# Optimization experiments

Hardware: AMD Instinct MI355X
Metric: run time of the kernel (lower is better)

Reference implementation:

```python
import jax, jax.numpy as jnp
import numpy as np

NH = 5   # num_multiheads (forced by the 5 gamma parameters)
FH = 64  # filters_head == in_dim (forced by residual broadcast)


def setup_inputs() -> dict:
    key = jax.random.key(0)
    k1, k2, k3 = jax.random.split(key, 3)
    B, C, D, H, W = 4, FH, 8, 64, 64
    x = jax.random.normal(k1, (B, C, D, H, W), dtype=jnp.float32)
    # pointwise qkv projection (stand-in for RBF_modified2d): in_dim -> 3*NH*FH
    Wqkv = jax.random.normal(k2, (3 * NH * FH, C), dtype=jnp.float32) * 0.02
    bqkv = jnp.zeros((3 * NH * FH,), dtype=jnp.float32)
    # gammas init to zeros in torch; use random values so attention path contributes
    gamma = jax.random.uniform(k3, (NH,), dtype=jnp.float32)
    return {"x": x, "Wqkv": Wqkv, "bqkv": bqkv, "gamma": gamma}


def reference(x, Wqkv, bqkv, gamma):
    B, C, D, H, W = x.shape
    # pointwise projection: (B, 3*NH*FH, D, H, W)
    qkv = jnp.einsum('bcdhw,oc->bodhw', x, Wqkv) + bqkv[None, :, None, None, None]
    # 'b (nh c) d h w -> b nh c d h w' with c = 3*FH, then chunk into q,k,v
    qkv = qkv.reshape(B, NH, 3 * FH, D, H, W)
    q, k, v = qkv[:, :, :FH], qkv[:, :, FH:2 * FH], qkv[:, :, 2 * FH:]
    # sim = k @ q^T over the last two (spatial) dims: (b,nh,c,d,H,H)
    sim = jnp.einsum('bncdiw,bncdjw->bncdij', k, q)
    att = jax.nn.softmax(sim, axis=-1)
    # att @ v -> (b, nh, c, d, H, W)
    pv = jnp.einsum('bncdij,bncdjw->bncdiw', att, v)
    # rearrange 'b nh c d h w -> b (c nh) d h w'
    out_att = pv.transpose(0, 2, 1, 3, 4, 5).reshape(B, FH * NH, D, H, W)
    # chunk into NH heads along merged channel axis -> (B, NH, FH, D, H, W)
    heads = out_att.reshape(B, NH, FH, D, H, W)
    # stack([gamma_i * head_i + x for i]) -> (NH, B, C, D, H, W)
    result = gamma[None, :, None, None, None, None] * heads + x[:, None]
    # rearrange 'nh b c d h w -> b (c nh) d h w'
    result = result.transpose(0, 2, 1, 3, 4, 5)  # (B, C, NH, D, H, W)
    return result.reshape(B, C * NH, D, H, W)
```

## Files before the change

### kernel.cpp

```cpp
#include <hip/hip_runtime.h>
#include <hip/hip_bf16.h>

typedef __bf16 bf16x8 __attribute__((ext_vector_type(8)));
typedef float  f32x4  __attribute__((ext_vector_type(4)));

#define NHEAD 5
#define FHD   64

__global__ __launch_bounds__(256) void k0_xpose(const float* __restrict__ x,
                                                __bf16* __restrict__ xbf,
                                                int slice_base) {
  int blk = blockIdx.x;
  int ls = blk >> 4;
  int pt = blk & 15;
  int g  = slice_base + ls;
  int b = g >> 3, d = g & 7;
  __shared__ __attribute__((aligned(16))) float xs[64][257];
  const int t = threadIdx.x;
  const int wv = t >> 6, l = t & 63;
  const float* xbase = x + (((size_t)b * 64) * 8 + d) * 4096 + pt * 256;
  for (int i = 0; i < 16; ++i) {
    int row = i * 4 + wv;
    int col = l * 4;
    float4 v = *(const float4*)(xbase + (size_t)row * 32768 + col);
    xs[row][col + 0] = v.x; xs[row][col + 1] = v.y;
    xs[row][col + 2] = v.z; xs[row][col + 3] = v.w;
  }
  __syncthreads();
  for (int i = 0; i < 8; ++i) {
    int chunk = i * 256 + t;
    int p = chunk >> 3, cb = chunk & 7;
    bf16x8 o;
    for (int j = 0; j < 8; ++j) o[j] = (__bf16)xs[cb * 8 + j][p];
    *(bf16x8*)(xbf + ((size_t)ls * 4096 + pt * 256 + p) * 64 + cb * 8) = o;
  }
}

__global__ __launch_bounds__(256) void k1_qkv(const __bf16* __restrict__ xbf,
                                              const float* __restrict__ W,
                                              const float* __restrict__ bias,
                                              __bf16* __restrict__ qkv,
                                              int slice_base) {
  int blk = blockIdx.x;
  int ls = blk / 240;
  int r  = blk % 240;
  int ot = r >> 4;
  int pt = r & 15;
  int o0 = ot * 64;
  __shared__ __attribute__((aligned(16))) __bf16 wlds[64 * 72];
  __shared__ float blds[64];
  __shared__ __attribute__((aligned(16))) __bf16 xt[256 * 72];
  const int t = threadIdx.x;
  for (int i = 0; i < 4; ++i) {
    int e = i * 1024 + t * 4;
    int row = e >> 6, col = e & 63;
    float4 v = *(const float4*)(W + (size_t)o0 * 64 + e);
    __bf16* dst = wlds + row * 72 + col;
    dst[0] = (__bf16)v.x; dst[1] = (__bf16)v.y; dst[2] = (__bf16)v.z; dst[3] = (__bf16)v.w;
  }
  if (t < 64) blds[t] = bias[o0 + t];
  const __bf16* xsrc = xbf + (size_t)ls * 262144 + (size_t)pt * 16384;
  for (int i = 0; i < 8; ++i) {
    int e = (i * 256 + t) * 8;
    int p = e >> 6, c0 = e & 63;
    *(bf16x8*)(xt + p * 72 + c0) = *(const bf16x8*)(xsrc + e);
  }
  __syncthreads();
  const int wv = t >> 6, l = t & 63;
  const int lr = l & 15, g4 = l >> 4;
  const f32x4 zero4 = {0.f, 0.f, 0.f, 0.f};
  bf16x8 a0 = *(const bf16x8*)(wlds + (16 * wv + lr) * 72 + g4 * 8);
  bf16x8 a1 = *(const bf16x8*)(wlds + (16 * wv + lr) * 72 + 32 + g4 * 8);
  f32x4 acc[16];
  for (int i = 0; i < 16; ++i) acc[i] = zero4;
  for (int p2 = 0; p2 < 16; ++p2) {
    const __bf16* xrow = xt + (p2 * 16 + lr) * 72 + g4 * 8;
    bf16x8 b0 = *(const bf16x8*)(xrow);
    bf16x8 b1 = *(const bf16x8*)(xrow + 32);
    acc[p2] = __builtin_amdgcn_mfma_f32_16x16x32_bf16(a0, b0, acc[p2], 0, 0, 0);
    acc[p2] = __builtin_amdgcn_mfma_f32_16x16x32_bf16(a1, b1, acc[p2], 0, 0, 0);
  }
  float bv[4];
  for (int rr = 0; rr < 4; ++rr) bv[rr] = blds[16 * wv + 4 * g4 + rr];
  __syncthreads();
  __bf16* rp = xt;
  for (int p2 = 0; p2 < 16; ++p2)
    for (int rr = 0; rr < 4; ++rr) {
      int o_l = 16 * wv + 4 * g4 + rr;
      rp[o_l * 264 + p2 * 16 + lr] = (__bf16)(acc[p2][rr] + bv[rr]);
    }
  __syncthreads();
  for (int i = 0; i < 8; ++i) {
    int chunk = i * 256 + t;
    int row = chunk >> 5, cb = chunk & 31;
    bf16x8 v = *(const bf16x8*)(rp + row * 264 + cb * 8);
    *(bf16x8*)(qkv + ((size_t)ls * 960 + o0 + row) * 4096 + (size_t)pt * 256 + cb * 8) = v;
  }
}

__global__ __launch_bounds__(256) void k2_attn(const __bf16* __restrict__ qkv,
                                               const float* __restrict__ x,
                                               const float* __restrict__ gamma,
                                               float* __restrict__ out,
                                               int slice_base) {
  int blk = blockIdx.x;
  int ls = blk / 320;
  int r  = blk % 320;
  int n  = r >> 6;
  int c  = r & 63;
  int g = slice_base + ls;
  int b = g >> 3, d = g & 7;
  __shared__ __attribute__((aligned(16))) __bf16 qlds[64 * 72];
  __shared__ __attribute__((aligned(16))) __bf16 klds[64 * 72];
  __shared__ __attribute__((aligned(16))) __bf16 vt[64 * 72];
  __shared__ __attribute__((aligned(16))) __bf16 attl[64 * 72];
  const int t = threadIdx.x;
  const __bf16* qp = qkv + ((size_t)ls * 960 + n * 192 + c) * 4096;
  const __bf16* kp = qp + (size_t)64 * 4096;
  const __bf16* vp = qp + (size_t)128 * 4096;
  {
    int row = t >> 2, c0 = (t & 3) * 16;
    *(bf16x8*)(qlds + row * 72 + c0)     = *(const bf16x8*)(qp + row * 64 + c0);
    *(bf16x8*)(qlds + row * 72 + c0 + 8) = *(const bf16x8*)(qp + row * 64 + c0 + 8);
    *(bf16x8*)(klds + row * 72 + c0)     = *(const bf16x8*)(kp + row * 64 + c0);
    *(bf16x8*)(klds + row * 72 + c0 + 8) = *(const bf16x8*)(kp + row * 64 + c0 + 8);
    bf16x8 v0 = *(const bf16x8*)(vp + row * 64 + c0);
    bf16x8 v1 = *(const bf16x8*)(vp + row * 64 + c0 + 8);
    for (int i = 0; i < 8; ++i) vt[(c0 + i) * 72 + row]     = v0[i];
    for (int i = 0; i < 8; ++i) vt[(c0 + 8 + i) * 72 + row] = v1[i];
  }
  __syncthreads();
  const int wv = t >> 6, l = t & 63;
  const int lr = l & 15, g4 = l >> 4;
  const int i0 = wv * 16;
  const f32x4 zero4 = {0.f, 0.f, 0.f, 0.f};
  f32x4 sacc[4];
  for (int i = 0; i < 4; ++i) sacc[i] = zero4;
  {
    bf16x8 a0 = *(const bf16x8*)(klds + (i0 + lr) * 72 + g4 * 8);
    bf16x8 a1 = *(const bf16x8*)(klds + (i0 + lr) * 72 + 32 + g4 * 8);
    for (int jt = 0; jt < 4; ++jt) {
      bf16x8 b0 = *(const bf16x8*)(qlds + (jt * 16 + lr) * 72 + g4 * 8);
      bf16x8 b1 = *(const bf16x8*)(qlds + (jt * 16 + lr) * 72 + 32 + g4 * 8);
      sacc[jt] = __builtin_amdgcn_mfma_f32_16x16x32_bf16(a0, b0, sacc[jt], 0, 0, 0);
      sacc[jt] = __builtin_amdgcn_mfma_f32_16x16x32_bf16(a1, b1, sacc[jt], 0, 0, 0);
    }
  }
  float pr[4][4];
  for (int rr = 0; rr < 4; ++rr) {
    float m = fmaxf(fmaxf(sacc[0][rr], sacc[1][rr]), fmaxf(sacc[2][rr], sacc[3][rr]));
    for (int dd = 1; dd < 16; dd <<= 1) m = fmaxf(m, __shfl_xor(m, dd));
    float s = 0.f;
    for (int jt = 0; jt < 4; ++jt) { pr[jt][rr] = __expf(sacc[jt][rr] - m); s += pr[jt][rr]; }
    for (int dd = 1; dd < 16; dd <<= 1) s += __shfl_xor(s, dd);
    float inv = 1.0f / s;
    for (int jt = 0; jt < 4; ++jt) pr[jt][rr] *= inv;
  }
  for (int jt = 0; jt < 4; ++jt)
    for (int rr = 0; rr < 4; ++rr)
      attl[(i0 + 4 * g4 + rr) * 72 + jt * 16 + lr] = (__bf16)pr[jt][rr];
  __syncthreads();
  f32x4 pv[4];
  for (int i = 0; i < 4; ++i) pv[i] = zero4;
  {
    bf16x8 a0 = *(const bf16x8*)(attl + (i0 + lr) * 72 + g4 * 8);
    bf16x8 a1 = *(const bf16x8*)(attl + (i0 + lr) * 72 + 32 + g4 * 8);
    for (int wt = 0; wt < 4; ++wt) {
      bf16x8 b0 = *(const bf16x8*)(vt + (wt * 16 + lr) * 72 + g4 * 8);
      bf16x8 b1 = *(const bf16x8*)(vt + (wt * 16 + lr) * 72 + 32 + g4 * 8);
      pv[wt] = __builtin_amdgcn_mfma_f32_16x16x32_bf16(a0, b0, pv[wt], 0, 0, 0);
      pv[wt] = __builtin_amdgcn_mfma_f32_16x16x32_bf16(a1, b1, pv[wt], 0, 0, 0);
    }
  }
  int o2 = c * NHEAD + n;
  int np = o2 >> 6, fp = o2 & 63;
  int oc = fp * NHEAD + np;
  float gm = gamma[np];
  const float* xp = x + (((size_t)b * 64 + fp) * 8 + d) * 4096;
  float* op = out + (((size_t)b * 320 + oc) * 8 + d) * 4096;
  for (int wt = 0; wt < 4; ++wt)
    for (int rr = 0; rr < 4; ++rr) {
      int i = i0 + 4 * g4 + rr;
      int w = wt * 16 + lr;
      int idx = i * 64 + w;
      op[idx] = gm * pv[wt][rr] + xp[idx];
    }
}

extern "C" void kernel_launch(void* const* d_in, const int* in_sizes, int n_in,
                              void* d_out, int out_size, void* d_ws, size_t ws_size,
                              hipStream_t stream) {
  const float* x     = (const float*)d_in[0];
  const float* W     = (const float*)d_in[1];
  const float* bias  = (const float*)d_in[2];
  const float* gamma = (const float*)d_in[3];
  float* out = (float*)d_out;

  const size_t per_slice = 524288 + 7864320;
  int S = (int)(ws_size / per_slice);
  if (S > 32) S = 32;
  if (S < 1)  S = 1;
  __bf16* xbf = (__bf16*)d_ws;
  __bf16* qkv = (__bf16*)((char*)d_ws + (size_t)S * 524288);

  for (int sb = 0; sb < 32; sb += S) {
    int sc = 32 - sb; if (sc > S) sc = S;
    k0_xpose<<<16  * sc, 256, 0, stream>>>(x, xbf, sb);
    k1_qkv  <<<240 * sc, 256, 0, stream>>>(xbf, W, bias, qkv, sb);
    k2_attn <<<320 * sc, 256, 0, stream>>>(qkv, x, gamma, out, sb);
  }
}
```

Before: 172.7 us.

## Fuse QKV projection into attention kernel, removing qkv workspace round-trip

Merges the pointwise QKV projection and the per-channel attention into one 512-thread kernel. Each block computes q, k and v for 4 channels of one head straight into XOR-swizzled LDS, then runs softmax attention for those channels. This removes the large bf16 qkv write and re-read through global memory, and one kernel launch per slice. It adds a block-index remap for locality. The cost is that 16-row MFMA tiles are padded from 12 real rows, so a quarter of projection compute is wasted, and each block now holds much more LDS.

```diff
diff --git a/kernel.cpp b/kernel.cpp
--- a/kernel.cpp
+++ b/kernel.cpp
@@ -5,7 +5,6 @@
 typedef float  f32x4  __attribute__((ext_vector_type(4)));
 
 #define NHEAD 5
-#define FHD   64
 
 __global__ __launch_bounds__(256) void k0_xpose(const float* __restrict__ x,
                                                 __bf16* __restrict__ xbf,
@@ -36,155 +35,185 @@
   }
 }
 
-__global__ __launch_bounds__(256) void k1_qkv(const __bf16* __restrict__ xbf,
-                                              const float* __restrict__ W,
-                                              const float* __restrict__ bias,
-                                              __bf16* __restrict__ qkv,
-                                              int slice_base) {
-  int blk = blockIdx.x;
-  int ls = blk / 240;
-  int r  = blk % 240;
-  int ot = r >> 4;
-  int pt = r & 15;
-  int o0 = ot * 64;
-  __shared__ __attribute__((aligned(16))) __bf16 wlds[64 * 72];
-  __shared__ float blds[64];
-  __shared__ __attribute__((aligned(16))) __bf16 xt[256 * 72];
-  const int t = threadIdx.x;
-  for (int i = 0; i < 4; ++i) {
-    int e = i * 1024 + t * 4;
-    int row = e >> 6, col = e & 63;
-    float4 v = *(const float4*)(W + (size_t)o0 * 64 + e);
-    __bf16* dst = wlds + row * 72 + col;
-    dst[0] = (__bf16)v.x; dst[1] = (__bf16)v.y; dst[2] = (__bf16)v.z; dst[3] = (__bf16)v.w;
-  }
-  if (t < 64) blds[t] = bias[o0 + t];
-  const __bf16* xsrc = xbf + (size_t)ls * 262144 + (size_t)pt * 16384;
-  for (int i = 0; i < 8; ++i) {
-    int e = (i * 256 + t) * 8;
-    int p = e >> 6, c0 = e & 63;
-    *(bf16x8*)(xt + p * 72 + c0) = *(const bf16x8*)(xsrc + e);
-  }
-  __syncthreads();
-  const int wv = t >> 6, l = t & 63;
-  const int lr = l & 15, g4 = l >> 4;
-  const f32x4 zero4 = {0.f, 0.f, 0.f, 0.f};
-  bf16x8 a0 = *(const bf16x8*)(wlds + (16 * wv + lr) * 72 + g4 * 8);
-  bf16x8 a1 = *(const bf16x8*)(wlds + (16 * wv + lr) * 72 + 32 + g4 * 8);
-  f32x4 acc[16];
-  for (int i = 0; i < 16; ++i) acc[i] = zero4;
-  for (int p2 = 0; p2 < 16; ++p2) {
-    const __bf16* xrow = xt + (p2 * 16 + lr) * 72 + g4 * 8;
-    bf16x8 b0 = *(const bf16x8*)(xrow);
-    bf16x8 b1 = *(const bf16x8*)(xrow + 32);
-    acc[p2] = __builtin_amdgcn_mfma_f32_16x16x32_bf16(a0, b0, acc[p2], 0, 0, 0);
-    acc[p2] = __builtin_amdgcn_mfma_f32_16x16x32_bf16(a1, b1, acc[p2], 0, 0, 0);
-  }
-  float bv[4];
-  for (int rr = 0; rr < 4; ++rr) bv[rr] = blds[16 * wv + 4 * g4 + rr];
-  __syncthreads();
-  __bf16* rp = xt;
-  for (int p2 = 0; p2 < 16; ++p2)
-    for (int rr = 0; rr < 4; ++rr) {
-      int o_l = 16 * wv + 4 * g4 + rr;
-      rp[o_l * 264 + p2 * 16 + lr] = (__bf16)(acc[p2][rr] + bv[rr]);
-    }
-  __syncthreads();
-  for (int i = 0; i < 8; ++i) {
-    int chunk = i * 256 + t;
-    int row = chunk >> 5, cb = chunk & 31;
-    bf16x8 v = *(const bf16x8*)(rp + row * 264 + cb * 8);
-    *(bf16x8*)(qkv + ((size_t)ls * 960 + o0 + row) * 4096 + (size_t)pt * 256 + cb * 8) = v;
-  }
-}
-
-__global__ __launch_bounds__(256) void k2_attn(const __bf16* __restrict__ qkv,
-                                               const float* __restrict__ x,
-                                               const float* __restrict__ gamma,
-                                               float* __restrict__ out,
-                                               int slice_base) {
-  int blk = blockIdx.x;
-  int ls = blk / 320;
-  int r  = blk % 320;
-  int n  = r >> 6;
-  int c  = r & 63;
+__global__ __launch_bounds__(512) void k1_fused(const __bf16* __restrict__ xbf,
+                                                const float* __restrict__ x,
+                                                const float* __restrict__ W,
+                                                const float* __restrict__ bias,
+                                                const float* __restrict__ gamma,
+                                                float* __restrict__ out,
+                                                int slice_base) {
+  __shared__ __attribute__((aligned(16))) __bf16 wl[16 * 72];
+  __shared__ float blds[32];
+  __shared__ __attribute__((aligned(16))) __bf16 qk[8][4096];
+  __shared__ __attribute__((aligned(16))) __bf16 vt[4][64 * 72];
+  __shared__ __attribute__((aligned(16))) __bf16 att[4][4096];
+
+  int nwg = gridDim.x;
+  int bid = blockIdx.x;
+  int nb = (bid & 7) * (nwg >> 3) + (bid >> 3);
+  int ls = nb / 80;
+  int r  = nb % 80;
+  int n  = r >> 4;
+  int c0 = (r & 15) * 4;
   int g = slice_base + ls;
   int b = g >> 3, d = g & 7;
-  __shared__ __attribute__((aligned(16))) __bf16 qlds[64 * 72];
-  __shared__ __attribute__((aligned(16))) __bf16 klds[64 * 72];
-  __shared__ __attribute__((aligned(16))) __bf16 vt[64 * 72];
-  __shared__ __attribute__((aligned(16))) __bf16 attl[64 * 72];
+
   const int t = threadIdx.x;
-  const __bf16* qp = qkv + ((size_t)ls * 960 + n * 192 + c) * 4096;
-  const __bf16* kp = qp + (size_t)64 * 4096;
-  const __bf16* vp = qp + (size_t)128 * 4096;
-  {
-    int row = t >> 2, c0 = (t & 3) * 16;
-    *(bf16x8*)(qlds + row * 72 + c0)     = *(const bf16x8*)(qp + row * 64 + c0);
-    *(bf16x8*)(qlds + row * 72 + c0 + 8) = *(const bf16x8*)(qp + row * 64 + c0 + 8);
-    *(bf16x8*)(klds + row * 72 + c0)     = *(const bf16x8*)(kp + row * 64 + c0);
-    *(bf16x8*)(klds + row * 72 + c0 + 8) = *(const bf16x8*)(kp + row * 64 + c0 + 8);
-    bf16x8 v0 = *(const bf16x8*)(vp + row * 64 + c0);
-    bf16x8 v1 = *(const bf16x8*)(vp + row * 64 + c0 + 8);
-    for (int i = 0; i < 8; ++i) vt[(c0 + i) * 72 + row]     = v0[i];
-    for (int i = 0; i < 8; ++i) vt[(c0 + 8 + i) * 72 + row] = v1[i];
-  }
-  __syncthreads();
-  const int wv = t >> 6, l = t & 63;
-  const int lr = l & 15, g4 = l >> 4;
-  const int i0 = wv * 16;
+  const int wv = t >> 6, l = t & 63, lr = l & 15, g4 = l >> 4;
+
+  for (int e = t; e < 1024; e += 512) {
+    int row = e >> 6, c = e & 63;
+    float v = 0.f;
+    if (row < 12) v = W[(size_t)(n * 192 + (row >> 2) * 64 + c0 + (row & 3)) * 64 + c];
+    wl[row * 72 + c] = (__bf16)v;
+  }
+  if (t < 16) blds[t] = (t < 12) ? bias[n * 192 + (t >> 2) * 64 + c0 + (t & 3)] : 0.f;
+  __syncthreads();
+
+  bf16x8 wa0 = *(const bf16x8*)(wl + lr * 72 + g4 * 8);
+  bf16x8 wa1 = *(const bf16x8*)(wl + lr * 72 + 32 + g4 * 8);
+  float bv[4];
+  for (int rr = 0; rr < 4; ++rr) bv[rr] = blds[4 * g4 + rr];
+
+  const __bf16* xs = xbf + (size_t)ls * 262144;
   const f32x4 zero4 = {0.f, 0.f, 0.f, 0.f};
-  f32x4 sacc[4];
-  for (int i = 0; i < 4; ++i) sacc[i] = zero4;
-  {
-    bf16x8 a0 = *(const bf16x8*)(klds + (i0 + lr) * 72 + g4 * 8);
-    bf16x8 a1 = *(const bf16x8*)(klds + (i0 + lr) * 72 + 32 + g4 * 8);
-    for (int jt = 0; jt < 4; ++jt) {
-      bf16x8 b0 = *(const bf16x8*)(qlds + (jt * 16 + lr) * 72 + g4 * 8);
-      bf16x8 b1 = *(const bf16x8*)(qlds + (jt * 16 + lr) * 72 + 32 + g4 * 8);
-      sacc[jt] = __builtin_amdgcn_mfma_f32_16x16x32_bf16(a0, b0, sacc[jt], 0, 0, 0);
-      sacc[jt] = __builtin_amdgcn_mfma_f32_16x16x32_bf16(a1, b1, sacc[jt], 0, 0, 0);
-    }
-  }
-  float pr[4][4];
-  for (int rr = 0; rr < 4; ++rr) {
-    float m = fmaxf(fmaxf(sacc[0][rr], sacc[1][rr]), fmaxf(sacc[2][rr], sacc[3][rr]));
-    for (int dd = 1; dd < 16; dd <<= 1) m = fmaxf(m, __shfl_xor(m, dd));
-    float s = 0.f;
-    for (int jt = 0; jt < 4; ++jt) { pr[jt][rr] = __expf(sacc[jt][rr] - m); s += pr[jt][rr]; }
-    for (int dd = 1; dd < 16; dd <<= 1) s += __shfl_xor(s, dd);
-    float inv = 1.0f / s;
-    for (int jt = 0; jt < 4; ++jt) pr[jt][rr] *= inv;
-  }
-  for (int jt = 0; jt < 4; ++jt)
-    for (int rr = 0; rr < 4; ++rr)
-      attl[(i0 + 4 * g4 + rr) * 72 + jt * 16 + lr] = (__bf16)pr[jt][rr];
-  __syncthreads();
-  f32x4 pv[4];
-  for (int i = 0; i < 4; ++i) pv[i] = zero4;
-  {
-    bf16x8 a0 = *(const bf16x8*)(attl + (i0 + lr) * 72 + g4 * 8);
-    bf16x8 a1 = *(const bf16x8*)(attl + (i0 + lr) * 72 + 32 + g4 * 8);
-    for (int wt = 0; wt < 4; ++wt) {
-      bf16x8 b0 = *(const bf16x8*)(vt + (wt * 16 + lr) * 72 + g4 * 8);
-      bf16x8 b1 = *(const bf16x8*)(vt + (wt * 16 + lr) * 72 + 32 + g4 * 8);
-      pv[wt] = __builtin_amdgcn_mfma_f32_16x16x32_bf16(a0, b0, pv[wt], 0, 0, 0);
-      pv[wt] = __builtin_amdgcn_mfma_f32_16x16x32_bf16(a1, b1, pv[wt], 0, 0, 0);
-    }
-  }
+
+  for (int h = 0; h < 2; ++h) {
+    int pbase = wv * 512 + h * 256;
+    f32x4 acc[16];
+#pragma unroll
+    for (int f = 0; f < 16; ++f) acc[f] = zero4;
+#pragma unroll
+    for (int f = 0; f < 16; ++f) {
+      const __bf16* bp = xs + (size_t)(pbase + f * 16 + lr) * 64;
+      bf16x8 b0 = *(const bf16x8*)(bp + g4 * 8);
+      bf16x8 b1 = *(const bf16x8*)(bp + 32 + g4 * 8);
+      acc[f] = __builtin_amdgcn_mfma_f32_16x16x32_bf16(wa0, b0, acc[f], 0, 0, 0);
+      acc[f] = __builtin_amdgcn_mfma_f32_16x16x32_bf16(wa1, b1, acc[f], 0, 0, 0);
+    }
+#pragma unroll
+    for (int f = 0; f < 16; ++f) {
+      int p = pbase + f * 16 + lr;
+      int i = p >> 6, w = p & 63;
+      if (g4 == 0) {
+#pragma unroll
+        for (int rr = 0; rr < 4; ++rr)
+          qk[rr][(i * 64 + w) ^ ((i & 7) << 3)] = (__bf16)(acc[f][rr] + bv[rr]);
+      } else if (g4 == 1) {
+#pragma unroll
+        for (int rr = 0; rr < 4; ++rr)
+          qk[4 + rr][(i * 64 + w) ^ ((i & 7) << 3)] = (__bf16)(acc[f][rr] + bv[rr]);
+      } else if (g4 == 2) {
+#pragma unroll
+        for (int rr = 0; rr < 4; ++rr)
+          vt[rr][w * 72 + i] = (__bf16)(acc[f][rr] + bv[rr]);
+      }
+    }
+  }
+  __syncthreads();
+
+  const int cl = wv >> 1;
+  const int i0 = (wv & 1) * 32;
+
+  f32x4 sacc[2][4];
+#pragma unroll
+  for (int ii = 0; ii < 2; ++ii)
+#pragma unroll
+    for (int jt = 0; jt < 4; ++jt) sacc[ii][jt] = zero4;
+  bf16x8 ka[2][2];
+#pragma unroll
+  for (int ii = 0; ii < 2; ++ii) {
+    int ia = i0 + ii * 16 + lr;
+    ka[ii][0] = *(const bf16x8*)(&qk[4 + cl][(ia * 64 + g4 * 8) ^ ((ia & 7) << 3)]);
+    ka[ii][1] = *(const bf16x8*)(&qk[4 + cl][(ia * 64 + 32 + g4 * 8) ^ ((ia & 7) << 3)]);
+  }
+#pragma unroll
+  for (int jt = 0; jt < 4; ++jt) {
+    int ja = jt * 16 + lr;
+    bf16x8 qb0 = *(const bf16x8*)(&qk[cl][(ja * 64 + g4 * 8) ^ ((ja & 7) << 3)]);
+    bf16x8 qb1 = *(const bf16x8*)(&qk[cl][(ja * 64 + 32 + g4 * 8) ^ ((ja & 7) << 3)]);
+#pragma unroll
+    for (int ii = 0; ii < 2; ++ii) {
+      sacc[ii][jt] = __builtin_amdgcn_mfma_f32_16x16x32_bf16(ka[ii][0], qb0, sacc[ii][jt], 0, 0, 0);
+      sacc[ii][jt] = __builtin_amdgcn_mfma_f32_16x16x32_bf16(ka[ii][1], qb1, sacc[ii][jt], 0, 0, 0);
+    }
+  }
+
+  float pr[2][4][4];
+#pragma unroll
+  for (int ii = 0; ii < 2; ++ii)
+#pragma unroll
+    for (int rr = 0; rr < 4; ++rr) {
+      float m = fmaxf(fmaxf(sacc[ii][0][rr], sacc[ii][1][rr]),
+                      fmaxf(sacc[ii][2][rr], sacc[ii][3][rr]));
+#pragma unroll
+      for (int dd = 1; dd < 16; dd <<= 1) m = fmaxf(m, __shfl_xor(m, dd));
+      float s = 0.f;
+#pragma unroll
+      for (int jt = 0; jt < 4; ++jt) {
+        pr[ii][jt][rr] = __expf(sacc[ii][jt][rr] - m);
+        s += pr[ii][jt][rr];
+      }
+#pragma unroll
+      for (int dd = 1; dd < 16; dd <<= 1) s += __shfl_xor(s, dd);
+      float inv = 1.0f / s;
+#pragma unroll
+      for (int jt = 0; jt < 4; ++jt) pr[ii][jt][rr] *= inv;
+    }
+
+#pragma unroll
+  for (int ii = 0; ii < 2; ++ii)
+#pragma unroll
+    for (int jt = 0; jt < 4; ++jt)
+#pragma unroll
+      for (int rr = 0; rr < 4; ++rr) {
+        int i = i0 + ii * 16 + 4 * g4 + rr;
+        int j = jt * 16 + lr;
+        att[cl][(i * 64 + j) ^ ((i & 7) << 3)] = (__bf16)pr[ii][jt][rr];
+      }
+  __syncthreads();
+
+  f32x4 pacc[2][4];
+#pragma unroll
+  for (int ii = 0; ii < 2; ++ii)
+#pragma unroll
+    for (int wt = 0; wt < 4; ++wt) pacc[ii][wt] = zero4;
+  bf16x8 aa[2][2];
+#pragma unroll
+  for (int ii = 0; ii < 2; ++ii) {
+    int ia = i0 + ii * 16 + lr;
+    aa[ii][0] = *(const bf16x8*)(&att[cl][(ia * 64 + g4 * 8) ^ ((ia & 7) << 3)]);
+    aa[ii][1] = *(const bf16x8*)(&att[cl][(ia * 64 + 32 + g4 * 8) ^ ((ia & 7) << 3)]);
+  }
+#pragma unroll
+  for (int wt = 0; wt < 4; ++wt) {
+    bf16x8 vb0 = *(const bf16x8*)(&vt[cl][(wt * 16 + lr) * 72 + g4 * 8]);
+    bf16x8 vb1 = *(const bf16x8*)(&vt[cl][(wt * 16 + lr) * 72 + 32 + g4 * 8]);
+#pragma unroll
+    for (int ii = 0; ii < 2; ++ii) {
+      pacc[ii][wt] = __builtin_amdgcn_mfma_f32_16x16x32_bf16(aa[ii][0], vb0, pacc[ii][wt], 0, 0, 0);
+      pacc[ii][wt] = __builtin_amdgcn_mfma_f32_16x16x32_bf16(aa[ii][1], vb1, pacc[ii][wt], 0, 0, 0);
+    }
+  }
+
+  int c = c0 + cl;
   int o2 = c * NHEAD + n;
   int np = o2 >> 6, fp = o2 & 63;
   int oc = fp * NHEAD + np;
   float gm = gamma[np];
   const float* xp = x + (((size_t)b * 64 + fp) * 8 + d) * 4096;
   float* op = out + (((size_t)b * 320 + oc) * 8 + d) * 4096;
-  for (int wt = 0; wt < 4; ++wt)
-    for (int rr = 0; rr < 4; ++rr) {
-      int i = i0 + 4 * g4 + rr;
-      int w = wt * 16 + lr;
-      int idx = i * 64 + w;
-      op[idx] = gm * pv[wt][rr] + xp[idx];
-    }
+#pragma unroll
+  for (int ii = 0; ii < 2; ++ii)
+#pragma unroll
+    for (int wt = 0; wt < 4; ++wt)
+#pragma unroll
+      for (int rr = 0; rr < 4; ++rr) {
+        int i = i0 + ii * 16 + 4 * g4 + rr;
+        int w = wt * 16 + lr;
+        int idx = i * 64 + w;
+        op[idx] = gm * pacc[ii][wt][rr] + xp[idx];
+      }
 }
 
 extern "C" void kernel_launch(void* const* d_in, const int* in_sizes, int n_in,
@@ -196,17 +225,14 @@
   const float* gamma = (const float*)d_in[3];
   float* out = (float*)d_out;
 
-  const size_t per_slice = 524288 + 7864320;
-  int S = (int)(ws_size / per_slice);
+  int S = (int)(ws_size / 524288);
   if (S > 32) S = 32;
   if (S < 1)  S = 1;
   __bf16* xbf = (__bf16*)d_ws;
-  __bf16* qkv = (__bf16*)((char*)d_ws + (size_t)S * 524288);
 
   for (int sb = 0; sb < 32; sb += S) {
     int sc = 32 - sb; if (sc > S) sc = S;
-    k0_xpose<<<16  * sc, 256, 0, stream>>>(x, xbf, sb);
-    k1_qkv  <<<240 * sc, 256, 0, stream>>>(xbf, W, bias, qkv, sb);
-    k2_attn <<<320 * sc, 256, 0, stream>>>(qkv, x, gamma, out, sb);
+    k0_xpose<<<16 * sc, 256, 0, stream>>>(x, xbf, sb);
+    k1_fused<<<80 * sc, 512, 0, stream>>>(xbf, x, W, bias, gamma, out, sb);
   }
 }
```

New measurement: 284.2 us. 64.5% more time.

## Process four channels per attention block with double-buffered LDS prefetch

Applied to the files above, without the earlier changes.

The attention kernel now handles four (channel) slices per block instead of one, cutting the grid from 320 to 80 blocks per slice. Global loads of the next q/k/v tile are issued into registers while the current tile is computed, and the residual x is prefetched. LDS switches from padded rows to XOR-swizzled layouts, and the output is staged through LDS so each thread writes contiguous float4 stores. The goal is to hide load latency and coalesce the output writes. The cost is fewer blocks in flight, more barriers per block, and higher register pressure under the occupancy hint.

```diff
diff --git a/kernel.cpp b/kernel.cpp
--- a/kernel.cpp
+++ b/kernel.cpp
@@ -5,7 +5,6 @@
 typedef float  f32x4  __attribute__((ext_vector_type(4)));
 
 #define NHEAD 5
-#define FHD   64
 
 __global__ __launch_bounds__(256) void k0_xpose(const float* __restrict__ x,
                                                 __bf16* __restrict__ xbf,
@@ -98,93 +97,190 @@
   }
 }
 
-__global__ __launch_bounds__(256) void k2_attn(const __bf16* __restrict__ qkv,
-                                               const float* __restrict__ x,
-                                               const float* __restrict__ gamma,
-                                               float* __restrict__ out,
-                                               int slice_base) {
-  int blk = blockIdx.x;
-  int ls = blk / 320;
-  int r  = blk % 320;
-  int n  = r >> 6;
-  int c  = r & 63;
+__global__ __launch_bounds__(256, 3) void k2_attn(const __bf16* __restrict__ qkv,
+                                                  const float* __restrict__ x,
+                                                  const float* __restrict__ gamma,
+                                                  float* __restrict__ out,
+                                                  int slice_base) {
+  __shared__ __attribute__((aligned(16))) __bf16 buf[2][3][4096];
+  int nb = blockIdx.x;
+  int ls = nb / 80;
+  int r  = nb % 80;
+  int n  = r >> 4;
+  int cg = r & 15;
   int g = slice_base + ls;
   int b = g >> 3, d = g & 7;
-  __shared__ __attribute__((aligned(16))) __bf16 qlds[64 * 72];
-  __shared__ __attribute__((aligned(16))) __bf16 klds[64 * 72];
-  __shared__ __attribute__((aligned(16))) __bf16 vt[64 * 72];
-  __shared__ __attribute__((aligned(16))) __bf16 attl[64 * 72];
+
   const int t = threadIdx.x;
-  const __bf16* qp = qkv + ((size_t)ls * 960 + n * 192 + c) * 4096;
-  const __bf16* kp = qp + (size_t)64 * 4096;
-  const __bf16* vp = qp + (size_t)128 * 4096;
-  {
-    int row = t >> 2, c0 = (t & 3) * 16;
-    *(bf16x8*)(qlds + row * 72 + c0)     = *(const bf16x8*)(qp + row * 64 + c0);
-    *(bf16x8*)(qlds + row * 72 + c0 + 8) = *(const bf16x8*)(qp + row * 64 + c0 + 8);
-    *(bf16x8*)(klds + row * 72 + c0)     = *(const bf16x8*)(kp + row * 64 + c0);
-    *(bf16x8*)(klds + row * 72 + c0 + 8) = *(const bf16x8*)(kp + row * 64 + c0 + 8);
-    bf16x8 v0 = *(const bf16x8*)(vp + row * 64 + c0);
-    bf16x8 v1 = *(const bf16x8*)(vp + row * 64 + c0 + 8);
-    for (int i = 0; i < 8; ++i) vt[(c0 + i) * 72 + row]     = v0[i];
-    for (int i = 0; i < 8; ++i) vt[(c0 + 8 + i) * 72 + row] = v1[i];
-  }
-  __syncthreads();
-  const int wv = t >> 6, l = t & 63;
-  const int lr = l & 15, g4 = l >> 4;
+  const int wv = t >> 6, l = t & 63, lr = l & 15, g4 = l >> 4;
   const int i0 = wv * 16;
+  const int srow = t >> 2;
+  const int scol = (t & 3) * 16;
   const f32x4 zero4 = {0.f, 0.f, 0.f, 0.f};
-  f32x4 sacc[4];
-  for (int i = 0; i < 4; ++i) sacc[i] = zero4;
-  {
-    bf16x8 a0 = *(const bf16x8*)(klds + (i0 + lr) * 72 + g4 * 8);
-    bf16x8 a1 = *(const bf16x8*)(klds + (i0 + lr) * 72 + 32 + g4 * 8);
+
+  const __bf16* base = qkv + (size_t)(ls * 960 + n * 192 + cg * 4) * 4096;
+
+  bf16x8 rq0, rq1, rk0, rk1, rv0, rv1;
+  f32x4 xpre[4];
+
+#define LOADA(A)                                                        \
+  {                                                                     \
+    const __bf16* qp = base + (size_t)(A) * 4096;                       \
+    const __bf16* kp = qp + (size_t)64 * 4096;                          \
+    const __bf16* vp = qp + (size_t)128 * 4096;                         \
+    rq0 = *(const bf16x8*)(qp + srow * 64 + scol);                      \
+    rq1 = *(const bf16x8*)(qp + srow * 64 + scol + 8);                  \
+    rk0 = *(const bf16x8*)(kp + srow * 64 + scol);                      \
+    rk1 = *(const bf16x8*)(kp + srow * 64 + scol + 8);                  \
+    rv0 = *(const bf16x8*)(vp + srow * 64 + scol);                      \
+    rv1 = *(const bf16x8*)(vp + srow * 64 + scol + 8);                  \
+  }
+
+#define STOREA(CUR)                                                     \
+  {                                                                     \
+    int a0 = (srow * 64 + scol) ^ ((srow & 7) << 3);                    \
+    int a1 = (srow * 64 + scol + 8) ^ ((srow & 7) << 3);                \
+    *(bf16x8*)(&buf[CUR][0][a0]) = rq0;                                 \
+    *(bf16x8*)(&buf[CUR][0][a1]) = rq1;                                 \
+    *(bf16x8*)(&buf[CUR][1][a0]) = rk0;                                 \
+    *(bf16x8*)(&buf[CUR][1][a1]) = rk1;                                 \
+    for (int kk = 0; kk < 8; ++kk) {                                    \
+      int w0 = scol + kk, w1 = scol + 8 + kk;                           \
+      buf[CUR][2][(w0 * 64 + srow) ^ ((w0 & 7) << 3)] = rv0[kk];        \
+      buf[CUR][2][(w1 * 64 + srow) ^ ((w1 & 7) << 3)] = rv1[kk];        \
+    }                                                                   \
+  }
+
+#define PREFX(A)                                                        \
+  {                                                                     \
+    int o2 = (cg * 4 + (A)) * NHEAD + n;                                \
+    int fp = o2 & 63;                                                   \
+    const float* xp = x + (((size_t)b * 64 + fp) * 8 + d) * 4096 + t * 16; \
+    xpre[0] = *(const f32x4*)(xp);                                      \
+    xpre[1] = *(const f32x4*)(xp + 4);                                  \
+    xpre[2] = *(const f32x4*)(xp + 8);                                  \
+    xpre[3] = *(const f32x4*)(xp + 12);                                 \
+  }
+
+  LOADA(0)
+  STOREA(0)
+  PREFX(0)
+  __syncthreads();
+
+  for (int a = 0; a < 4; ++a) {
+    const int cur = a & 1;
+    if (a < 3) LOADA(a + 1)
+
+    f32x4 sacc[4];
+#pragma unroll
+    for (int jt = 0; jt < 4; ++jt) sacc[jt] = zero4;
+    bf16x8 ka0, ka1;
+    {
+      int ia = i0 + lr;
+      ka0 = *(const bf16x8*)(&buf[cur][1][(ia * 64 + g4 * 8) ^ ((ia & 7) << 3)]);
+      ka1 = *(const bf16x8*)(&buf[cur][1][(ia * 64 + 32 + g4 * 8) ^ ((ia & 7) << 3)]);
+    }
+#pragma unroll
     for (int jt = 0; jt < 4; ++jt) {
-      bf16x8 b0 = *(const bf16x8*)(qlds + (jt * 16 + lr) * 72 + g4 * 8);
-      bf16x8 b1 = *(const bf16x8*)(qlds + (jt * 16 + lr) * 72 + 32 + g4 * 8);
-      sacc[jt] = __builtin_amdgcn_mfma_f32_16x16x32_bf16(a0, b0, sacc[jt], 0, 0, 0);
-      sacc[jt] = __builtin_amdgcn_mfma_f32_16x16x32_bf16(a1, b1, sacc[jt], 0, 0, 0);
-    }
-  }
-  float pr[4][4];
-  for (int rr = 0; rr < 4; ++rr) {
-    float m = fmaxf(fmaxf(sacc[0][rr], sacc[1][rr]), fmaxf(sacc[2][rr], sacc[3][rr]));
-    for (int dd = 1; dd < 16; dd <<= 1) m = fmaxf(m, __shfl_xor(m, dd));
-    float s = 0.f;
-    for (int jt = 0; jt < 4; ++jt) { pr[jt][rr] = __expf(sacc[jt][rr] - m); s += pr[jt][rr]; }
-    for (int dd = 1; dd < 16; dd <<= 1) s += __shfl_xor(s, dd);
-    float inv = 1.0f / s;
-    for (int jt = 0; jt < 4; ++jt) pr[jt][rr] *= inv;
-  }
-  for (int jt = 0; jt < 4; ++jt)
-    for (int rr = 0; rr < 4; ++rr)
-      attl[(i0 + 4 * g4 + rr) * 72 + jt * 16 + lr] = (__bf16)pr[jt][rr];
-  __syncthreads();
-  f32x4 pv[4];
-  for (int i = 0; i < 4; ++i) pv[i] = zero4;
-  {
-    bf16x8 a0 = *(const bf16x8*)(attl + (i0 + lr) * 72 + g4 * 8);
-    bf16x8 a1 = *(const bf16x8*)(attl + (i0 + lr) * 72 + 32 + g4 * 8);
+      int ja = jt * 16 + lr;
+      bf16x8 qb0 = *(const bf16x8*)(&buf[cur][0][(ja * 64 + g4 * 8) ^ ((ja & 7) << 3)]);
+      bf16x8 qb1 = *(const bf16x8*)(&buf[cur][0][(ja * 64 + 32 + g4 * 8) ^ ((ja & 7) << 3)]);
+      sacc[jt] = __builtin_amdgcn_mfma_f32_16x16x32_bf16(ka0, qb0, sacc[jt], 0, 0, 0);
+      sacc[jt] = __builtin_amdgcn_mfma_f32_16x16x32_bf16(ka1, qb1, sacc[jt], 0, 0, 0);
+    }
+
+    float pr[4][4];
+#pragma unroll
+    for (int rr = 0; rr < 4; ++rr) {
+      float m = fmaxf(fmaxf(sacc[0][rr], sacc[1][rr]), fmaxf(sacc[2][rr], sacc[3][rr]));
+#pragma unroll
+      for (int dd = 1; dd < 16; dd <<= 1) m = fmaxf(m, __shfl_xor(m, dd));
+      float s = 0.f;
+#pragma unroll
+      for (int jt = 0; jt < 4; ++jt) {
+        pr[jt][rr] = __expf(sacc[jt][rr] - m);
+        s += pr[jt][rr];
+      }
+#pragma unroll
+      for (int dd = 1; dd < 16; dd <<= 1) s += __shfl_xor(s, dd);
+      float inv = 1.0f / s;
+#pragma unroll
+      for (int jt = 0; jt < 4; ++jt) pr[jt][rr] *= inv;
+    }
+    __syncthreads();
+
+#pragma unroll
+    for (int jt = 0; jt < 4; ++jt)
+#pragma unroll
+      for (int rr = 0; rr < 4; ++rr) {
+        int i = i0 + 4 * g4 + rr;
+        int j = jt * 16 + lr;
+        buf[cur][1][(i * 64 + j) ^ ((i & 7) << 3)] = (__bf16)pr[jt][rr];
+      }
+    __syncthreads();
+
+    f32x4 pacc[4];
+#pragma unroll
+    for (int wt = 0; wt < 4; ++wt) pacc[wt] = zero4;
+    bf16x8 aa0, aa1;
+    {
+      int ia = i0 + lr;
+      aa0 = *(const bf16x8*)(&buf[cur][1][(ia * 64 + g4 * 8) ^ ((ia & 7) << 3)]);
+      aa1 = *(const bf16x8*)(&buf[cur][1][(ia * 64 + 32 + g4 * 8) ^ ((ia & 7) << 3)]);
+    }
+#pragma unroll
     for (int wt = 0; wt < 4; ++wt) {
-      bf16x8 b0 = *(const bf16x8*)(vt + (wt * 16 + lr) * 72 + g4 * 8);
-      bf16x8 b1 = *(const bf16x8*)(vt + (wt * 16 + lr) * 72 + 32 + g4 * 8);
-      pv[wt] = __builtin_amdgcn_mfma_f32_16x16x32_bf16(a0, b0, pv[wt], 0, 0, 0);
-      pv[wt] = __builtin_amdgcn_mfma_f32_16x16x32_bf16(a1, b1, pv[wt], 0, 0, 0);
-    }
-  }
-  int o2 = c * NHEAD + n;
-  int np = o2 >> 6, fp = o2 & 63;
-  int oc = fp * NHEAD + np;
-  float gm = gamma[np];
-  const float* xp = x + (((size_t)b * 64 + fp) * 8 + d) * 4096;
-  float* op = out + (((size_t)b * 320 + oc) * 8 + d) * 4096;
-  for (int wt = 0; wt < 4; ++wt)
-    for (int rr = 0; rr < 4; ++rr) {
-      int i = i0 + 4 * g4 + rr;
-      int w = wt * 16 + lr;
-      int idx = i * 64 + w;
-      op[idx] = gm * pv[wt][rr] + xp[idx];
-    }
+      int wrow = wt * 16 + lr;
+      bf16x8 vb0 = *(const bf16x8*)(&buf[cur][2][(wrow * 64 + g4 * 8) ^ ((wrow & 7) << 3)]);
+      bf16x8 vb1 = *(const bf16x8*)(&buf[cur][2][(wrow * 64 + 32 + g4 * 8) ^ ((wrow & 7) << 3)]);
+      pacc[wt] = __builtin_amdgcn_mfma_f32_16x16x32_bf16(aa0, vb0, pacc[wt], 0, 0, 0);
+      pacc[wt] = __builtin_amdgcn_mfma_f32_16x16x32_bf16(aa1, vb1, pacc[wt], 0, 0, 0);
+    }
+    __syncthreads();
+
+    if (a < 3) STOREA(cur ^ 1)
+
+    float* fb = (float*)&buf[cur][0][0];
+#pragma unroll
+    for (int wt = 0; wt < 4; ++wt)
+#pragma unroll
+      for (int rr = 0; rr < 4; ++rr) {
+        int i = i0 + 4 * g4 + rr;
+        int w = wt * 16 + lr;
+        fb[(i * 64 + w) ^ ((i & 7) << 2)] = pacc[wt][rr];
+      }
+    __syncthreads();
+
+    {
+      int o2 = (cg * 4 + a) * NHEAD + n;
+      int np = o2 >> 6, fp = o2 & 63;
+      int oc = fp * NHEAD + np;
+      float gm = gamma[np];
+      int ib = t >> 2;
+      int xs_ = ((ib & 7) << 2);
+      f32x4 p0 = *(const f32x4*)(fb + ((t * 16 + 0) ^ xs_));
+      f32x4 p1 = *(const f32x4*)(fb + ((t * 16 + 4) ^ xs_));
+      f32x4 p2 = *(const f32x4*)(fb + ((t * 16 + 8) ^ xs_));
+      f32x4 p3 = *(const f32x4*)(fb + ((t * 16 + 12) ^ xs_));
+      f32x4 o0, o1, o2v, o3;
+#pragma unroll
+      for (int j = 0; j < 4; ++j) {
+        o0[j] = gm * p0[j] + xpre[0][j];
+        o1[j] = gm * p1[j] + xpre[1][j];
+        o2v[j] = gm * p2[j] + xpre[2][j];
+        o3[j] = gm * p3[j] + xpre[3][j];
+      }
+      float* op = out + (((size_t)b * 320 + oc) * 8 + d) * 4096 + t * 16;
+      *(f32x4*)(op + 0) = o0;
+      *(f32x4*)(op + 4) = o1;
+      *(f32x4*)(op + 8) = o2v;
+      *(f32x4*)(op + 12) = o3;
+    }
+    if (a < 3) PREFX(a + 1)
+  }
+#undef LOADA
+#undef STOREA
+#undef PREFX
 }
 
 extern "C" void kernel_launch(void* const* d_in, const int* in_sizes, int n_in,
@@ -207,6 +303,6 @@
     int sc = 32 - sb; if (sc > S) sc = S;
     k0_xpose<<<16  * sc, 256, 0, stream>>>(x, xbf, sb);
     k1_qkv  <<<240 * sc, 256, 0, stream>>>(xbf, W, bias, qkv, sb);
-    k2_attn <<<320 * sc, 256, 0, stream>>>(qkv, x, gamma, out, sb);
+    k2_attn <<<80  * sc, 256, 0, stream>>>(qkv, x, gamma, out, sb);
   }
 }
```

Measured after the change: 196.8 us. 13.9% more time.
